# Performance work log

Hardware: AMD Instinct MI355X
Metric: run time of the kernel (lower is better)

## Reference

```python
import jax, jax.numpy as jnp
import numpy as np

B, HF, WF = 64, 14, 14
E, D, H, EM, V, L = 2048, 256, 256, 256, 10000, 32


def setup_inputs() -> dict:
    key = jax.random.key(0)
    ks = jax.random.split(key, 16)
    s = lambda k, shape: jax.random.normal(k, shape, jnp.float32) * 0.02
    lengths = jnp.clip(jax.random.randint(ks[2], (B, 1), 2, L + 1), 2, L)
    lengths = lengths.at[0, 0].set(L)  # ensure max target length == L-1 (static)
    return {
        "image_feature": jax.random.normal(ks[0], (B, HF, WF, E), jnp.float32),
        "caption_token": jax.random.randint(ks[1], (B, L), 0, V),
        "caption_length": lengths,
        "Wf": s(ks[3], (E, H)), "bf": jnp.zeros((H,), jnp.float32),
        "Wh": s(ks[4], (D, H)), "bh": jnp.zeros((H,), jnp.float32),
        "We": s(ks[5], (H, 1)), "be": jnp.zeros((1,), jnp.float32),
        "emb": jax.random.uniform(ks[6], (V, EM), jnp.float32, -0.1, 0.1),
        "W_ih": s(ks[7], (EM + E, 4 * D)), "b_ih": jnp.zeros((4 * D,), jnp.float32),
        "W_hh": s(ks[8], (D, 4 * D)), "b_hh": jnp.zeros((4 * D,), jnp.float32),
        "W_hid": s(ks[9], (E, D)), "b_hid": jnp.zeros((D,), jnp.float32),
        "W_cell": s(ks[10], (E, D)), "b_cell": jnp.zeros((D,), jnp.float32),
        "W_gate": s(ks[11], (D, E)), "b_gate": jnp.zeros((E,), jnp.float32),
        "W_head": jax.random.uniform(ks[12], (D, V), jnp.float32, -0.1, 0.1),
        "b_head": jnp.zeros((V,), jnp.float32),
    }


def reference(image_feature, caption_token, caption_length,
              Wf, bf, Wh, bh, We, be, emb,
              W_ih, b_ih, W_hh, b_hh,
              W_hid, b_hid, W_cell, b_cell,
              W_gate, b_gate, W_head, b_head):
    feat = image_feature.reshape(image_feature.shape[0], -1, image_feature.shape[-1])  # [B,P,E]
    lengths = caption_length[:, 0]
    order = jnp.argsort(-lengths)               # descending, stable
    feat = feat[order]
    tok = caption_token[order]
    target = lengths[order] - 1                 # [B] target lengths
    T = tok.shape[1] - 1                        # static max target length

    mean_feat = feat.mean(axis=1)               # [B,E]
    h0 = mean_feat @ W_hid + b_hid              # init hidden
    c0 = mean_feat @ W_cell + b_cell            # init cell
    cap_emb = emb[tok]                          # [B,L,EM] teacher-forcing embeds
    fe = feat @ Wf + bf                         # [B,P,H] feature proj (loop-invariant)

    def step(carry, t):
        h, c = carry
        m = (target > t)[:, None].astype(h.dtype)        # active-row mask (block_size)
        # additive attention
        he = (h @ Wh + bh)[:, None, :]                   # [B,1,H]
        e = jax.nn.relu(fe + he) @ We + be               # [B,P,1]
        w = jax.nn.softmax(e, axis=1)                    # over pixels
        ctx = (w * feat).sum(axis=1)                     # [B,E]
        # sigmoid gate on context
        ctx = jax.nn.sigmoid(h @ W_gate + b_gate) * ctx
        # LSTMCell (torch gate order i,f,g,o)
        x = jnp.concatenate([cap_emb[:, t], ctx], axis=1)
        g = x @ W_ih + b_ih + h @ W_hh + b_hh
        i, f, gg, o = jnp.split(g, 4, axis=1)
        c_new = jax.nn.sigmoid(f) * c + jax.nn.sigmoid(i) * jnp.tanh(gg)
        h_new = jax.nn.sigmoid(o) * jnp.tanh(c_new)
        pred = h_new @ W_head + b_head                   # dropout = identity (eval)
        h = jnp.where(m > 0, h_new, h)
        c = jnp.where(m > 0, c_new, c)
        return (h, c), (pred * m, w[:, :, 0] * m)

    _, (preds, weights) = jax.lax.scan(step, (h0, c0), jnp.arange(T))
    caption_prediction = jnp.transpose(preds, (1, 0, 2))   # [B,T,V]
    attention_weight = jnp.transpose(weights, (1, 0, 2))   # [B,T,P]
    return caption_prediction, attention_weight
```

## Files before the change

kernel.cpp:

```cpp
#include <hip/hip_runtime.h>
#include <math.h>

#define B 64
#define P 196
#define E 2048
#define D 256
#define H_ 256
#define EM 256
#define V 10000
#define L 32
#define T 31
#define KX 2560

__global__ __launch_bounds__(64) void sort_kernel(const int* __restrict__ clen,
                                                  int* __restrict__ order,
                                                  int* __restrict__ target) {
    __shared__ int len_s[B];
    int i = threadIdx.x;
    len_s[i] = clen[i];
    __syncthreads();
    int li = len_s[i];
    int rank = 0;
    for (int j = 0; j < B; ++j) {
        int lj = len_s[j];
        if (lj > li || (lj == li && j < i)) rank++;
    }
    order[rank] = i;
    target[rank] = li - 1;
}

__global__ __launch_bounds__(256) void mean_kernel(const float* __restrict__ feat,
                                                   const int* __restrict__ order,
                                                   float* __restrict__ mean_feat) {
    int b = blockIdx.x;
    int e = blockIdx.y * 256 + threadIdx.x;
    int src = order[b];
    const float* fp = feat + (size_t)src * P * E + e;
    float acc = 0.f;
    #pragma unroll 4
    for (int p = 0; p < P; ++p) acc += fp[(size_t)p * E];
    mean_feat[b * E + e] = acc * (1.0f / (float)P);
}

__global__ __launch_bounds__(256) void h0c0_gemm(const float* __restrict__ mean_feat,
                                                 const float* __restrict__ W_hid,
                                                 const float* __restrict__ W_cell,
                                                 float* __restrict__ hpart) {
    __shared__ float As[32][68];
    __shared__ float Bs[32][64];
    int cb = blockIdx.x;
    int ky = blockIdx.y;
    int tid = threadIdx.x;
    int tx = tid & 15, ty = tid >> 4;
    const float* Wsrc;
    int ncol0;
    if (cb < 4) { Wsrc = W_hid;  ncol0 = cb * 64; }
    else        { Wsrc = W_cell; ncol0 = (cb - 4) * 64; }
    float acc[4][4] = {};
    for (int k0 = ky * 256; k0 < ky * 256 + 256; k0 += 32) {
        #pragma unroll
        for (int q = 0; q < 2; ++q) {
            int idx = q * 256 + tid;
            int kv = idx & 7, m = idx >> 3;
            float4 v = *(const float4*)(mean_feat + (size_t)m * E + k0 + kv * 4);
            As[kv * 4 + 0][m] = v.x;
            As[kv * 4 + 1][m] = v.y;
            As[kv * 4 + 2][m] = v.z;
            As[kv * 4 + 3][m] = v.w;
        }
        #pragma unroll
        for (int q = 0; q < 2; ++q) {
            int idx = q * 256 + tid;
            int n4 = idx & 15, kk = idx >> 4;
            float4 v = *(const float4*)(Wsrc + (size_t)(k0 + kk) * 256 + ncol0 + n4 * 4);
            *(float4*)&Bs[kk][n4 * 4] = v;
        }
        __syncthreads();
        #pragma unroll
        for (int kk = 0; kk < 32; ++kk) {
            float4 av = *(const float4*)&As[kk][ty * 4];
            float4 bv = *(const float4*)&Bs[kk][tx * 4];
            acc[0][0] += av.x * bv.x; acc[0][1] += av.x * bv.y; acc[0][2] += av.x * bv.z; acc[0][3] += av.x * bv.w;
            acc[1][0] += av.y * bv.x; acc[1][1] += av.y * bv.y; acc[1][2] += av.y * bv.z; acc[1][3] += av.y * bv.w;
            acc[2][0] += av.z * bv.x; acc[2][1] += av.z * bv.y; acc[2][2] += av.z * bv.z; acc[2][3] += av.z * bv.w;
            acc[3][0] += av.w * bv.x; acc[3][1] += av.w * bv.y; acc[3][2] += av.w * bv.z; acc[3][3] += av.w * bv.w;
        }
        __syncthreads();
    }
    #pragma unroll
    for (int a = 0; a < 4; ++a) {
        int row = ty * 4 + a;
        float4 o = {acc[a][0], acc[a][1], acc[a][2], acc[a][3]};
        *(float4*)(hpart + ((size_t)ky * B + row) * 512 + cb * 64 + tx * 4) = o;
    }
}

__global__ __launch_bounds__(256) void h0c0_reduce(const float* __restrict__ hpart,
                                                   const float* __restrict__ b_hid,
                                                   const float* __restrict__ b_cell,
                                                   const float* __restrict__ emb,
                                                   const int* __restrict__ cap_tok,
                                                   const int* __restrict__ order,
                                                   float* __restrict__ h,
                                                   float* __restrict__ c,
                                                   float* __restrict__ xbuf) {
    int b = blockIdx.x, tid = threadIdx.x;
    float s0 = 0.f, s1 = 0.f;
    #pragma unroll
    for (int ky = 0; ky < 8; ++ky) {
        const float* hp = hpart + ((size_t)ky * B + b) * 512;
        s0 += hp[tid];
        s1 += hp[256 + tid];
    }
    float h0 = s0 + b_hid[tid];
    h[b * D + tid] = h0;
    c[b * D + tid] = s1 + b_cell[tid];
    xbuf[(size_t)b * KX + 2304 + tid] = h0;
    int tok0 = cap_tok[order[b] * L + 0];
    xbuf[(size_t)b * KX + tid] = emb[(size_t)tok0 * EM + tid];
}

__global__ __launch_bounds__(256) void fe_gemm(const float* __restrict__ feat,
                                               const int* __restrict__ order,
                                               const float* __restrict__ Wf,
                                               const float* __restrict__ bf,
                                               float* __restrict__ fe) {
    __shared__ float As[32][68];
    __shared__ float Bs[32][64];
    __shared__ int srcRow[64];
    int rowBlock = blockIdx.x;
    int colBlock = blockIdx.y;
    int tid = threadIdx.x;
    if (tid < 64) {
        int gr = rowBlock * 64 + tid;
        int b = gr / P, p = gr % P;
        srcRow[tid] = order[b] * P + p;
    }
    __syncthreads();
    int tx = tid & 15, ty = tid >> 4;
    float acc[4][4] = {};
    for (int k0 = 0; k0 < E; k0 += 32) {
        #pragma unroll
        for (int q = 0; q < 2; ++q) {
            int idx = q * 256 + tid;
            int kv = idx & 7, m = idx >> 3;
            float4 v = *(const float4*)(feat + (size_t)srcRow[m] * E + k0 + kv * 4);
            As[kv * 4 + 0][m] = v.x;
            As[kv * 4 + 1][m] = v.y;
            As[kv * 4 + 2][m] = v.z;
            As[kv * 4 + 3][m] = v.w;
        }
        {
            int n4 = tid & 15, kk = tid >> 4;
            float4 v = *(const float4*)(Wf + (size_t)(k0 + kk) * H_ + colBlock * 64 + n4 * 4);
            *(float4*)&Bs[kk][n4 * 4] = v;
            int kk2 = kk + 16;
            float4 v2 = *(const float4*)(Wf + (size_t)(k0 + kk2) * H_ + colBlock * 64 + n4 * 4);
            *(float4*)&Bs[kk2][n4 * 4] = v2;
        }
        __syncthreads();
        #pragma unroll
        for (int kk = 0; kk < 32; ++kk) {
            float4 av = *(const float4*)&As[kk][ty * 4];
            float4 bv = *(const float4*)&Bs[kk][tx * 4];
            acc[0][0] += av.x * bv.x; acc[0][1] += av.x * bv.y; acc[0][2] += av.x * bv.z; acc[0][3] += av.x * bv.w;
            acc[1][0] += av.y * bv.x; acc[1][1] += av.y * bv.y; acc[1][2] += av.y * bv.z; acc[1][3] += av.y * bv.w;
            acc[2][0] += av.z * bv.x; acc[2][1] += av.z * bv.y; acc[2][2] += av.z * bv.z; acc[2][3] += av.z * bv.w;
            acc[3][0] += av.w * bv.x; acc[3][1] += av.w * bv.y; acc[3][2] += av.w * bv.z; acc[3][3] += av.w * bv.w;
        }
        __syncthreads();
    }
    float4 bias = *(const float4*)(bf + colBlock * 64 + tx * 4);
    #pragma unroll
    for (int a = 0; a < 4; ++a) {
        int gr = rowBlock * 64 + ty * 4 + a;
        float4 o;
        o.x = acc[a][0] + bias.x;
        o.y = acc[a][1] + bias.y;
        o.z = acc[a][2] + bias.z;
        o.w = acc[a][3] + bias.w;
        *(float4*)(fe + (size_t)gr * H_ + colBlock * 64 + tx * 4) = o;
    }
}

__global__ __launch_bounds__(256) void attn_pw(const int* __restrict__ target,
                                               const float* __restrict__ gpart,
                                               const float* __restrict__ b_ih,
                                               const float* __restrict__ b_hh,
                                               const float* __restrict__ emb,
                                               const int* __restrict__ cap_tok,
                                               const int* __restrict__ order,
                                               const float* __restrict__ Wh,
                                               const float* __restrict__ bh,
                                               const float* __restrict__ We,
                                               const float* __restrict__ be,
                                               const float* __restrict__ fe,
                                               float* __restrict__ h,
                                               float* __restrict__ c,
                                               float* __restrict__ hn_all,
                                               float* __restrict__ xbuf,
                                               float* __restrict__ wbuf,
                                               float* __restrict__ out2,
                                               int t) {
    int b = blockIdx.x;
    int tgt = target[b];
    bool pw_active = (t > 0) && (tgt > t - 1);
    bool at_active = (tgt > t);
    if (!pw_active && !at_active) return;
    __shared__ float hs[D];
    __shared__ float hes[D];
    __shared__ float es[P];
    __shared__ float red[4];
    int tid = threadIdx.x;
    if (pw_active) {
        int d = tid;
        float gi = b_ih[d] + b_hh[d];
        float gf = b_ih[D + d] + b_hh[D + d];
        float gg = b_ih[2 * D + d] + b_hh[2 * D + d];
        float go = b_ih[3 * D + d] + b_hh[3 * D + d];
        #pragma unroll
        for (int ky = 0; ky < 8; ++ky) {
            const float* gp = gpart + ((size_t)ky * B + b) * 1024;
            gi += gp[d];
            gf += gp[D + d];
            gg += gp[2 * D + d];
            go += gp[3 * D + d];
        }
        float c_old = c[b * D + d];
        float si = 1.f / (1.f + expf(-gi));
        float sf = 1.f / (1.f + expf(-gf));
        float so = 1.f / (1.f + expf(-go));
        float cn = sf * c_old + si * tanhf(gg);
        float hnv = so * tanhf(cn);
        c[b * D + d] = cn;
        h[b * D + d] = hnv;
        hs[d] = hnv;
        hn_all[((size_t)(t - 1) * B + b) * D + d] = hnv;
        xbuf[(size_t)b * KX + 2304 + d] = hnv;
        int tokn = cap_tok[order[b] * L + t];
        xbuf[(size_t)b * KX + d] = emb[(size_t)tokn * EM + d];
    } else {
        hs[tid] = h[b * D + tid];
    }
    __syncthreads();
    if (!at_active) return;
    float acc = 0.f;
    #pragma unroll 8
    for (int k = 0; k < D; ++k) acc += hs[k] * Wh[(size_t)k * H_ + tid];
    hes[tid] = acc + bh[tid];
    __syncthreads();
    int wave = tid >> 6, lane = tid & 63;
    float4 he4 = *(const float4*)&hes[lane * 4];
    float4 we4 = *(const float4*)(We + lane * 4);
    for (int p = wave; p < P; p += 4) {
        float4 fv = *(const float4*)(fe + ((size_t)b * P + p) * H_ + lane * 4);
        float x0 = fv.x + he4.x; x0 = x0 > 0.f ? x0 : 0.f;
        float x1 = fv.y + he4.y; x1 = x1 > 0.f ? x1 : 0.f;
        float x2 = fv.z + he4.z; x2 = x2 > 0.f ? x2 : 0.f;
        float x3 = fv.w + he4.w; x3 = x3 > 0.f ? x3 : 0.f;
        float s = x0 * we4.x + x1 * we4.y + x2 * we4.z + x3 * we4.w;
        #pragma unroll
        for (int off = 32; off > 0; off >>= 1) s += __shfl_down(s, off);
        if (lane == 0) es[p] = s + be[0];
    }
    __syncthreads();
    float mx = -1e30f;
    for (int p = tid; p < P; p += 256) mx = fmaxf(mx, es[p]);
    #pragma unroll
    for (int off = 32; off > 0; off >>= 1) mx = fmaxf(mx, __shfl_down(mx, off));
    if (lane == 0) red[wave] = mx;
    __syncthreads();
    mx = fmaxf(fmaxf(red[0], red[1]), fmaxf(red[2], red[3]));
    __syncthreads();
    float sum = 0.f;
    for (int p = tid; p < P; p += 256) {
        float ex = expf(es[p] - mx);
        es[p] = ex;
        sum += ex;
    }
    #pragma unroll
    for (int off = 32; off > 0; off >>= 1) sum += __shfl_down(sum, off);
    if (lane == 0) red[wave] = sum;
    __syncthreads();
    sum = red[0] + red[1] + red[2] + red[3];
    float inv = 1.0f / sum;
    for (int p = tid; p < P; p += 256) {
        float wv = es[p] * inv;
        wbuf[b * P + p] = wv;
        out2[((size_t)b * T + t) * P + p] = wv;
    }
}

__global__ __launch_bounds__(256) void ctx_kernel(const float* __restrict__ feat,
                                                  const int* __restrict__ order,
                                                  const float* __restrict__ wbuf,
                                                  const float* __restrict__ W_gate,
                                                  const float* __restrict__ b_gate,
                                                  const float* __restrict__ h,
                                                  const int* __restrict__ target,
                                                  float* __restrict__ xbuf,
                                                  int t) {
    int b = blockIdx.x;
    if (target[b] <= t) return;
    int y = blockIdx.y;
    __shared__ float ws_[P];
    __shared__ float hs[D];
    __shared__ float4 rc[3][64];
    __shared__ float4 rg[3][64];
    int tid = threadIdx.x;
    if (tid < P) ws_[tid] = wbuf[b * P + tid];
    hs[tid] = h[b * D + tid];
    __syncthreads();
    int c4 = tid & 63, q = tid >> 6;
    int src = order[b];
    const float4* f4 = (const float4*)(feat + (size_t)src * P * E) + y * 64 + c4;
    float4 acc = {0.f, 0.f, 0.f, 0.f};
    for (int p = q * 49; p < q * 49 + 49; ++p) {
        float w = ws_[p];
        float4 fv = f4[(size_t)p * 512];
        acc.x += w * fv.x; acc.y += w * fv.y; acc.z += w * fv.z; acc.w += w * fv.w;
    }
    const float4* g4 = (const float4*)W_gate + y * 64 + c4;
    float4 gacc = {0.f, 0.f, 0.f, 0.f};
    for (int k = q * 64; k < q * 64 + 64; ++k) {
        float hv = hs[k];
        float4 wv = g4[(size_t)k * 512];
        gacc.x += hv * wv.x; gacc.y += hv * wv.y; gacc.z += hv * wv.z; gacc.w += hv * wv.w;
    }
    if (q) { rc[q - 1][c4] = acc; rg[q - 1][c4] = gacc; }
    __syncthreads();
    if (q == 0) {
        #pragma unroll
        for (int j = 0; j < 3; ++j) {
            float4 a = rc[j][c4], g = rg[j][c4];
            acc.x += a.x; acc.y += a.y; acc.z += a.z; acc.w += a.w;
            gacc.x += g.x; gacc.y += g.y; gacc.z += g.z; gacc.w += g.w;
        }
        float4 gb = *(const float4*)(b_gate + (y * 64 + c4) * 4);
        float4 o;
        o.x = acc.x / (1.f + expf(-(gacc.x + gb.x)));
        o.y = acc.y / (1.f + expf(-(gacc.y + gb.y)));
        o.z = acc.z / (1.f + expf(-(gacc.z + gb.z)));
        o.w = acc.w / (1.f + expf(-(gacc.w + gb.w)));
        *(float4*)(xbuf + (size_t)b * KX + EM + (y * 64 + c4) * 4) = o;
    }
}

__global__ __launch_bounds__(256) void lstm_gemm(const float* __restrict__ xbuf,
                                                 const float* __restrict__ W_ih,
                                                 const float* __restrict__ W_hh,
                                                 float* __restrict__ gpart) {
    __shared__ float As[32][68];
    __shared__ float Bs[32][64];
    int cb = blockIdx.x;
    int ky = blockIdx.y;
    int tid = threadIdx.x;
    int tx = tid & 15, ty = tid >> 4;
    float acc[4][4] = {};
    int k0base = ky * 320;
    for (int k0 = k0base; k0 < k0base + 320; k0 += 32) {
        #pragma unroll
        for (int q = 0; q < 2; ++q) {
            int idx = q * 256 + tid;
            int kv = idx & 7, m = idx >> 3;
            float4 v = *(const float4*)(xbuf + (size_t)m * KX + k0 + kv * 4);
            As[kv * 4 + 0][m] = v.x;
            As[kv * 4 + 1][m] = v.y;
            As[kv * 4 + 2][m] = v.z;
            As[kv * 4 + 3][m] = v.w;
        }
        #pragma unroll
        for (int q = 0; q < 2; ++q) {
            int idx = q * 256 + tid;
            int n4 = idx & 15, kk = idx >> 4;
            int k = k0 + kk;
            const float* src = (k < EM + E) ? (W_ih + (size_t)k * 1024)
                                            : (W_hh + (size_t)(k - EM - E) * 1024);
            float4 v = *(const float4*)(src + cb * 64 + n4 * 4);
            *(float4*)&Bs[kk][n4 * 4] = v;
        }
        __syncthreads();
        #pragma unroll
        for (int kk = 0; kk < 32; ++kk) {
            float4 av = *(const float4*)&As[kk][ty * 4];
            float4 bv = *(const float4*)&Bs[kk][tx * 4];
            acc[0][0] += av.x * bv.x; acc[0][1] += av.x * bv.y; acc[0][2] += av.x * bv.z; acc[0][3] += av.x * bv.w;
            acc[1][0] += av.y * bv.x; acc[1][1] += av.y * bv.y; acc[1][2] += av.y * bv.z; acc[1][3] += av.y * bv.w;
            acc[2][0] += av.z * bv.x; acc[2][1] += av.z * bv.y; acc[2][2] += av.z * bv.z; acc[2][3] += av.z * bv.w;
            acc[3][0] += av.w * bv.x; acc[3][1] += av.w * bv.y; acc[3][2] += av.w * bv.z; acc[3][3] += av.w * bv.w;
        }
        __syncthreads();
    }
    #pragma unroll
    for (int a = 0; a < 4; ++a) {
        int bidx = ty * 4 + a;
        float4 o = {acc[a][0], acc[a][1], acc[a][2], acc[a][3]};
        *(float4*)(gpart + ((size_t)ky * B + bidx) * 1024 + cb * 64 + tx * 4) = o;
    }
}

__global__ __launch_bounds__(256) void head_batch(const float* __restrict__ hn_all,
                                                  const float* __restrict__ W_head,
                                                  const float* __restrict__ b_head,
                                                  const int* __restrict__ target,
                                                  float* __restrict__ out1) {
    int by = blockIdx.y;
    int t = by >> 1, qh = by & 1;
    if (target[qh * 32] <= t) return;
    __shared__ float hs[32][260];
    int cb = blockIdx.x;
    int tid = threadIdx.x;
    #pragma unroll
    for (int q = 0; q < 8; ++q) {
        int idx = q * 256 + tid;
        int r = idx >> 6, kq = idx & 63;
        float4 v = *(const float4*)(hn_all + ((size_t)t * B + qh * 32 + r) * D + kq * 4);
        *(float4*)&hs[r][kq * 4] = v;
    }
    __syncthreads();
    int col = cb * 64 + (tid & 63);
    int rgrp = (tid >> 6) * 8;
    if (col < V) {
        float acc[8] = {};
        for (int kq = 0; kq < 64; ++kq) {
            float w0 = W_head[(size_t)(kq * 4 + 0) * V + col];
            float w1 = W_head[(size_t)(kq * 4 + 1) * V + col];
            float w2 = W_head[(size_t)(kq * 4 + 2) * V + col];
            float w3 = W_head[(size_t)(kq * 4 + 3) * V + col];
            #pragma unroll
            for (int r = 0; r < 8; ++r) {
                float4 hv = *(const float4*)&hs[rgrp + r][kq * 4];
                acc[r] += hv.x * w0 + hv.y * w1 + hv.z * w2 + hv.w * w3;
            }
        }
        float bh_ = b_head[col];
        #pragma unroll
        for (int r = 0; r < 8; ++r) {
            int brow = qh * 32 + rgrp + r;
            if (target[brow] > t)
                out1[((size_t)brow * T + t) * V + col] = acc[r] + bh_;
        }
    }
}

extern "C" void kernel_launch(void* const* d_in, const int* in_sizes, int n_in,
                              void* d_out, int out_size, void* d_ws, size_t ws_size,
                              hipStream_t stream) {
    const float* feat   = (const float*)d_in[0];
    const int*   tok    = (const int*)d_in[1];
    const int*   clen   = (const int*)d_in[2];
    const float* Wf     = (const float*)d_in[3];
    const float* bf     = (const float*)d_in[4];
    const float* Wh     = (const float*)d_in[5];
    const float* bh     = (const float*)d_in[6];
    const float* We     = (const float*)d_in[7];
    const float* be     = (const float*)d_in[8];
    const float* emb    = (const float*)d_in[9];
    const float* W_ih   = (const float*)d_in[10];
    const float* b_ih   = (const float*)d_in[11];
    const float* W_hh   = (const float*)d_in[12];
    const float* b_hh   = (const float*)d_in[13];
    const float* W_hid  = (const float*)d_in[14];
    const float* b_hid  = (const float*)d_in[15];
    const float* W_cell = (const float*)d_in[16];
    const float* b_cell = (const float*)d_in[17];
    const float* W_gate = (const float*)d_in[18];
    const float* b_gate = (const float*)d_in[19];
    const float* W_head = (const float*)d_in[20];
    const float* b_head = (const float*)d_in[21];

    float* out1 = (float*)d_out;
    float* out2 = out1 + (size_t)B * T * V;

    char* wp = (char*)d_ws;
    int* order   = (int*)wp;           wp += 256;
    int* targetp = (int*)wp;           wp += 256;
    float* fe    = (float*)wp;         wp += (size_t)B * P * H_ * sizeof(float);
    float* hbuf  = (float*)wp;         wp += (size_t)B * D * sizeof(float);
    float* cbuf  = (float*)wp;         wp += (size_t)B * D * sizeof(float);
    float* wbuf  = (float*)wp;         wp += (size_t)B * P * sizeof(float);
    float* xbuf  = (float*)wp;         wp += (size_t)B * KX * sizeof(float);
    float* gpart = (float*)wp;         wp += (size_t)8 * B * 1024 * sizeof(float);
    float* mean_feat = (float*)wp;     wp += (size_t)B * E * sizeof(float);
    float* hpart = (float*)wp;         wp += (size_t)8 * B * 512 * sizeof(float);
    float* hn_all = (float*)wp;        wp += (size_t)T * B * D * sizeof(float);

    hipMemsetAsync(d_out, 0, (size_t)out_size * sizeof(float), stream);

    sort_kernel<<<1, 64, 0, stream>>>(clen, order, targetp);
    mean_kernel<<<dim3(B, E / 256), 256, 0, stream>>>(feat, order, mean_feat);
    h0c0_gemm<<<dim3(8, 8), 256, 0, stream>>>(mean_feat, W_hid, W_cell, hpart);
    h0c0_reduce<<<B, 256, 0, stream>>>(hpart, b_hid, b_cell, emb, tok, order,
                                       hbuf, cbuf, xbuf);
    fe_gemm<<<dim3(196, 4), 256, 0, stream>>>(feat, order, Wf, bf, fe);

    for (int t = 0; t < T; ++t) {
        attn_pw<<<B, 256, 0, stream>>>(targetp, gpart, b_ih, b_hh, emb, tok, order,
                                       Wh, bh, We, be, fe, hbuf, cbuf, hn_all,
                                       xbuf, wbuf, out2, t);
        ctx_kernel<<<dim3(B, 8), 256, 0, stream>>>(feat, order, wbuf, W_gate, b_gate,
                                                   hbuf, targetp, xbuf, t);
        lstm_gemm<<<dim3(16, 8), 256, 0, stream>>>(xbuf, W_ih, W_hh, gpart);
    }
    attn_pw<<<B, 256, 0, stream>>>(targetp, gpart, b_ih, b_hh, emb, tok, order,
                                   Wh, bh, We, be, fe, hbuf, cbuf, hn_all,
                                   xbuf, wbuf, out2, T);
    head_batch<<<dim3(157, 62), 256, 0, stream>>>(hn_all, W_head, b_head, targetp, out1);
}
```

Before: 2.848 ms.

## Fuse recurrent time loop into one persistent cooperative kernel with grid syncs

Replaces the 94 per-timestep kernel launches (attention/pointwise, context, LSTM GEMM) with a single cooperative persistent kernel of 512 blocks that runs all phases and separates them with grid-wide barriers. This targets launch overhead and inter-kernel gaps in the latency-bound recurrence. It adds grid.sync costs, requires all 512 blocks to be co-resident, and keeps the old multi-launch path as a fallback if the cooperative launch fails.

```diff
diff --git a/kernel.cpp b/kernel.cpp
--- a/kernel.cpp
+++ b/kernel.cpp
@@ -1,5 +1,8 @@
 #include <hip/hip_runtime.h>
+#include <hip/hip_cooperative_groups.h>
 #include <math.h>
+
+namespace cg = cooperative_groups;
 
 #define B 64
 #define P 196
@@ -399,6 +402,227 @@
     }
 }
 
+__global__ __launch_bounds__(256, 2) void loop_kernel(
+        const int* __restrict__ target,
+        float* __restrict__ gpart,
+        const float* __restrict__ b_ih,
+        const float* __restrict__ b_hh,
+        const float* __restrict__ emb,
+        const int* __restrict__ cap_tok,
+        const int* __restrict__ order,
+        const float* __restrict__ Wh,
+        const float* __restrict__ bh,
+        const float* __restrict__ We,
+        const float* __restrict__ be,
+        const float* __restrict__ fe,
+        float* __restrict__ h,
+        float* __restrict__ c,
+        float* __restrict__ hn_all,
+        float* __restrict__ xbuf,
+        float* __restrict__ wbuf,
+        float* __restrict__ out2,
+        const float* __restrict__ feat,
+        const float* __restrict__ W_gate,
+        const float* __restrict__ b_gate,
+        const float* __restrict__ W_ih,
+        const float* __restrict__ W_hh) {
+    cg::grid_group grid = cg::this_grid();
+    __shared__ __align__(16) char smem_raw[17408];
+    int bid = blockIdx.x;
+    int tid = threadIdx.x;
+
+    for (int t = 0; ; ++t) {
+        if (bid < B) {
+            float* hs  = (float*)smem_raw;
+            float* hes = hs + 256;
+            float* es  = hes + 256;
+            float* red = es + 200;
+            int b = bid;
+            int tgt = target[b];
+            bool pw_active = (t > 0) && (tgt > t - 1);
+            bool at_active = (t < T) && (tgt > t);
+            if (pw_active || at_active) {
+                if (pw_active) {
+                    int d = tid;
+                    float gi = b_ih[d] + b_hh[d];
+                    float gf = b_ih[D + d] + b_hh[D + d];
+                    float gg = b_ih[2 * D + d] + b_hh[2 * D + d];
+                    float go = b_ih[3 * D + d] + b_hh[3 * D + d];
+                    #pragma unroll
+                    for (int ky = 0; ky < 8; ++ky) {
+                        const float* gp = gpart + ((size_t)ky * B + b) * 1024;
+                        gi += gp[d];
+                        gf += gp[D + d];
+                        gg += gp[2 * D + d];
+                        go += gp[3 * D + d];
+                    }
+                    float c_old = c[b * D + d];
+                    float si = 1.f / (1.f + expf(-gi));
+                    float sf = 1.f / (1.f + expf(-gf));
+                    float so = 1.f / (1.f + expf(-go));
+                    float cn = sf * c_old + si * tanhf(gg);
+                    float hnv = so * tanhf(cn);
+                    c[b * D + d] = cn;
+                    h[b * D + d] = hnv;
+                    hs[d] = hnv;
+                    hn_all[((size_t)(t - 1) * B + b) * D + d] = hnv;
+                    xbuf[(size_t)b * KX + 2304 + d] = hnv;
+                    int tokn = cap_tok[order[b] * L + t];
+                    xbuf[(size_t)b * KX + d] = emb[(size_t)tokn * EM + d];
+                } else {
+                    hs[tid] = h[b * D + tid];
+                }
+                __syncthreads();
+                if (at_active) {
+                    float acc = 0.f;
+                    #pragma unroll 8
+                    for (int k = 0; k < D; ++k) acc += hs[k] * Wh[(size_t)k * H_ + tid];
+                    hes[tid] = acc + bh[tid];
+                    __syncthreads();
+                    int wave = tid >> 6, lane = tid & 63;
+                    float4 he4 = *(const float4*)&hes[lane * 4];
+                    float4 we4 = *(const float4*)(We + lane * 4);
+                    for (int p = wave; p < P; p += 4) {
+                        float4 fv = *(const float4*)(fe + ((size_t)b * P + p) * H_ + lane * 4);
+                        float x0 = fv.x + he4.x; x0 = x0 > 0.f ? x0 : 0.f;
+                        float x1 = fv.y + he4.y; x1 = x1 > 0.f ? x1 : 0.f;
+                        float x2 = fv.z + he4.z; x2 = x2 > 0.f ? x2 : 0.f;
+                        float x3 = fv.w + he4.w; x3 = x3 > 0.f ? x3 : 0.f;
+                        float s = x0 * we4.x + x1 * we4.y + x2 * we4.z + x3 * we4.w;
+                        #pragma unroll
+                        for (int off = 32; off > 0; off >>= 1) s += __shfl_down(s, off);
+                        if (lane == 0) es[p] = s + be[0];
+                    }
+                    __syncthreads();
+                    float mx = -1e30f;
+                    for (int p = tid; p < P; p += 256) mx = fmaxf(mx, es[p]);
+                    #pragma unroll
+                    for (int off = 32; off > 0; off >>= 1) mx = fmaxf(mx, __shfl_down(mx, off));
+                    if (lane == 0) red[wave] = mx;
+                    __syncthreads();
+                    mx = fmaxf(fmaxf(red[0], red[1]), fmaxf(red[2], red[3]));
+                    __syncthreads();
+                    float sum = 0.f;
+                    for (int p = tid; p < P; p += 256) {
+                        float ex = expf(es[p] - mx);
+                        es[p] = ex;
+                        sum += ex;
+                    }
+                    #pragma unroll
+                    for (int off = 32; off > 0; off >>= 1) sum += __shfl_down(sum, off);
+                    if (lane == 0) red[wave] = sum;
+                    __syncthreads();
+                    sum = red[0] + red[1] + red[2] + red[3];
+                    float inv = 1.0f / sum;
+                    for (int p = tid; p < P; p += 256) {
+                        float wv = es[p] * inv;
+                        wbuf[b * P + p] = wv;
+                        out2[((size_t)b * T + t) * P + p] = wv;
+                    }
+                }
+            }
+        }
+        if (t == T) break;
+        grid.sync();
+
+        {
+            int b = bid >> 3, y = bid & 7;
+            if (target[b] > t) {
+                float*  ws_ = (float*)smem_raw;
+                float*  hsB = ws_ + 200;
+                float4* rc  = (float4*)(smem_raw + 1824);
+                float4* rg  = rc + 192;
+                if (tid < P) ws_[tid] = wbuf[b * P + tid];
+                hsB[tid] = h[b * D + tid];
+                __syncthreads();
+                int c4 = tid & 63, q = tid >> 6;
+                int src = order[b];
+                const float4* f4 = (const float4*)(feat + (size_t)src * P * E) + y * 64 + c4;
+                float4 acc = {0.f, 0.f, 0.f, 0.f};
+                for (int p = q * 49; p < q * 49 + 49; ++p) {
+                    float w = ws_[p];
+                    float4 fv = f4[(size_t)p * 512];
+                    acc.x += w * fv.x; acc.y += w * fv.y; acc.z += w * fv.z; acc.w += w * fv.w;
+                }
+                const float4* g4 = (const float4*)W_gate + y * 64 + c4;
+                float4 gacc = {0.f, 0.f, 0.f, 0.f};
+                for (int k = q * 64; k < q * 64 + 64; ++k) {
+                    float hv = hsB[k];
+                    float4 wv = g4[(size_t)k * 512];
+                    gacc.x += hv * wv.x; gacc.y += hv * wv.y; gacc.z += hv * wv.z; gacc.w += hv * wv.w;
+                }
+                if (q) { rc[(q - 1) * 64 + c4] = acc; rg[(q - 1) * 64 + c4] = gacc; }
+                __syncthreads();
+                if (q == 0) {
+                    #pragma unroll
+                    for (int j = 0; j < 3; ++j) {
+                        float4 a = rc[j * 64 + c4], g = rg[j * 64 + c4];
+                        acc.x += a.x; acc.y += a.y; acc.z += a.z; acc.w += a.w;
+                        gacc.x += g.x; gacc.y += g.y; gacc.z += g.z; gacc.w += g.w;
+                    }
+                    float4 gb = *(const float4*)(b_gate + (y * 64 + c4) * 4);
+                    float4 o;
+                    o.x = acc.x / (1.f + expf(-(gacc.x + gb.x)));
+                    o.y = acc.y / (1.f + expf(-(gacc.y + gb.y)));
+                    o.z = acc.z / (1.f + expf(-(gacc.z + gb.z)));
+                    o.w = acc.w / (1.f + expf(-(gacc.w + gb.w)));
+                    *(float4*)(xbuf + (size_t)b * KX + EM + (y * 64 + c4) * 4) = o;
+                }
+            }
+        }
+        grid.sync();
+
+        if (bid < 128) {
+            float (*As)[68] = (float (*)[68])smem_raw;
+            float (*Bs)[64] = (float (*)[64])(smem_raw + 8704);
+            int cb = bid & 15, ky = bid >> 4;
+            int tx = tid & 15, ty = tid >> 4;
+            float acc[4][4] = {};
+            int k0base = ky * 320;
+            for (int k0 = k0base; k0 < k0base + 320; k0 += 32) {
+                #pragma unroll
+                for (int q = 0; q < 2; ++q) {
+                    int idx = q * 256 + tid;
+                    int kv = idx & 7, m = idx >> 3;
+                    float4 v = *(const float4*)(xbuf + (size_t)m * KX + k0 + kv * 4);
+                    As[kv * 4 + 0][m] = v.x;
+                    As[kv * 4 + 1][m] = v.y;
+                    As[kv * 4 + 2][m] = v.z;
+                    As[kv * 4 + 3][m] = v.w;
+                }
+                #pragma unroll
+                for (int q = 0; q < 2; ++q) {
+                    int idx = q * 256 + tid;
+                    int n4 = idx & 15, kk = idx >> 4;
+                    int k = k0 + kk;
+                    const float* src = (k < EM + E) ? (W_ih + (size_t)k * 1024)
+                                                    : (W_hh + (size_t)(k - EM - E) * 1024);
+                    float4 v = *(const float4*)(src + cb * 64 + n4 * 4);
+                    *(float4*)&Bs[kk][n4 * 4] = v;
+                }
+                __syncthreads();
+                #pragma unroll
+                for (int kk = 0; kk < 32; ++kk) {
+                    float4 av = *(const float4*)&As[kk][ty * 4];
+                    float4 bv = *(const float4*)&Bs[kk][tx * 4];
+                    acc[0][0] += av.x * bv.x; acc[0][1] += av.x * bv.y; acc[0][2] += av.x * bv.z; acc[0][3] += av.x * bv.w;
+                    acc[1][0] += av.y * bv.x; acc[1][1] += av.y * bv.y; acc[1][2] += av.y * bv.z; acc[1][3] += av.y * bv.w;
+                    acc[2][0] += av.z * bv.x; acc[2][1] += av.z * bv.y; acc[2][2] += av.z * bv.z; acc[2][3] += av.z * bv.w;
+                    acc[3][0] += av.w * bv.x; acc[3][1] += av.w * bv.y; acc[3][2] += av.w * bv.z; acc[3][3] += av.w * bv.w;
+                }
+                __syncthreads();
+            }
+            #pragma unroll
+            for (int a = 0; a < 4; ++a) {
+                int bidx = ty * 4 + a;
+                float4 o = {acc[a][0], acc[a][1], acc[a][2], acc[a][3]};
+                *(float4*)(gpart + ((size_t)ky * B + bidx) * 1024 + cb * 64 + tx * 4) = o;
+            }
+        }
+        grid.sync();
+    }
+}
+
 __global__ __launch_bounds__(256) void head_batch(const float* __restrict__ hn_all,
                                                   const float* __restrict__ W_head,
                                                   const float* __restrict__ b_head,
@@ -494,16 +718,29 @@
                                        hbuf, cbuf, xbuf);
     fe_gemm<<<dim3(196, 4), 256, 0, stream>>>(feat, order, Wf, bf, fe);
 
-    for (int t = 0; t < T; ++t) {
+    void* kargs[] = {
+        (void*)&targetp, (void*)&gpart, (void*)&b_ih, (void*)&b_hh,
+        (void*)&emb, (void*)&tok, (void*)&order, (void*)&Wh, (void*)&bh,
+        (void*)&We, (void*)&be, (void*)&fe, (void*)&hbuf, (void*)&cbuf,
+        (void*)&hn_all, (void*)&xbuf, (void*)&wbuf, (void*)&out2,
+        (void*)&feat, (void*)&W_gate, (void*)&b_gate, (void*)&W_ih, (void*)&W_hh
+    };
+    hipError_t cerr = hipLaunchCooperativeKernel((const void*)loop_kernel,
+                                                 dim3(512), dim3(256),
+                                                 kargs, 0, stream);
+    if (cerr != hipSuccess) {
+        for (int t = 0; t < T; ++t) {
+            attn_pw<<<B, 256, 0, stream>>>(targetp, gpart, b_ih, b_hh, emb, tok, order,
+                                           Wh, bh, We, be, fe, hbuf, cbuf, hn_all,
+                                           xbuf, wbuf, out2, t);
+            ctx_kernel<<<dim3(B, 8), 256, 0, stream>>>(feat, order, wbuf, W_gate, b_gate,
+                                                       hbuf, targetp, xbuf, t);
+            lstm_gemm<<<dim3(16, 8), 256, 0, stream>>>(xbuf, W_ih, W_hh, gpart);
+        }
         attn_pw<<<B, 256, 0, stream>>>(targetp, gpart, b_ih, b_hh, emb, tok, order,
                                        Wh, bh, We, be, fe, hbuf, cbuf, hn_all,
-                                       xbuf, wbuf, out2, t);
-        ctx_kernel<<<dim3(B, 8), 256, 0, stream>>>(feat, order, wbuf, W_gate, b_gate,
-                                                   hbuf, targetp, xbuf, t);
-        lstm_gemm<<<dim3(16, 8), 256, 0, stream>>>(xbuf, W_ih, W_hh, gpart);
-    }
-    attn_pw<<<B, 256, 0, stream>>>(targetp, gpart, b_ih, b_hh, emb, tok, order,
-                                   Wh, bh, We, be, fe, hbuf, cbuf, hn_all,
-                                   xbuf, wbuf, out2, T);
+                                       xbuf, wbuf, out2, T);
+    }
+
     head_batch<<<dim3(157, 62), 256, 0, stream>>>(hn_all, W_head, b_head, targetp, out1);
 }
```

After: 10.61 ms. 273% more time.

## Fuse attention and context kernels per step with double-buffered cell state

Applied to the files above, without the earlier changes.

Merges the per-step attention/LSTM-pointwise kernel and the context/gate kernel into one kernel launched on a (batch, 8) grid. Each of the 8 column blocks recomputes the pointwise update, the Wh projection and the softmax so the attention weights stay in shared memory instead of going through a global buffer. The cell state is double-buffered across steps to avoid races between blocks, and a small final pointwise kernel replaces the last attention launch. This removes one launch and a global round-trip per step, but repeats the Wh matvec and the fe reads eight times per batch row.

```diff
diff --git a/kernel.cpp b/kernel.cpp
--- a/kernel.cpp
+++ b/kernel.cpp
@@ -102,7 +102,7 @@
                                                    const int* __restrict__ cap_tok,
                                                    const int* __restrict__ order,
                                                    float* __restrict__ h,
-                                                   float* __restrict__ c,
+                                                   float* __restrict__ c0,
                                                    float* __restrict__ xbuf) {
     int b = blockIdx.x, tid = threadIdx.x;
     float s0 = 0.f, s1 = 0.f;
@@ -114,7 +114,7 @@
     }
     float h0 = s0 + b_hid[tid];
     h[b * D + tid] = h0;
-    c[b * D + tid] = s1 + b_cell[tid];
+    c0[b * D + tid] = s1 + b_cell[tid];
     xbuf[(size_t)b * KX + 2304 + tid] = h0;
     int tok0 = cap_tok[order[b] * L + 0];
     xbuf[(size_t)b * KX + tid] = emb[(size_t)tok0 * EM + tid];
@@ -183,35 +183,41 @@
     }
 }
 
-__global__ __launch_bounds__(256) void attn_pw(const int* __restrict__ target,
-                                               const float* __restrict__ gpart,
-                                               const float* __restrict__ b_ih,
-                                               const float* __restrict__ b_hh,
-                                               const float* __restrict__ emb,
-                                               const int* __restrict__ cap_tok,
-                                               const int* __restrict__ order,
-                                               const float* __restrict__ Wh,
-                                               const float* __restrict__ bh,
-                                               const float* __restrict__ We,
-                                               const float* __restrict__ be,
-                                               const float* __restrict__ fe,
-                                               float* __restrict__ h,
-                                               float* __restrict__ c,
-                                               float* __restrict__ hn_all,
-                                               float* __restrict__ xbuf,
-                                               float* __restrict__ wbuf,
-                                               float* __restrict__ out2,
-                                               int t) {
-    int b = blockIdx.x;
+__global__ __launch_bounds__(256) void attn_ctx(const int* __restrict__ target,
+                                                const float* __restrict__ gpart,
+                                                const float* __restrict__ b_ih,
+                                                const float* __restrict__ b_hh,
+                                                const float* __restrict__ emb,
+                                                const int* __restrict__ cap_tok,
+                                                const int* __restrict__ order,
+                                                const float* __restrict__ Wh,
+                                                const float* __restrict__ bh,
+                                                const float* __restrict__ We,
+                                                const float* __restrict__ be,
+                                                const float* __restrict__ fe,
+                                                const float* __restrict__ h0,
+                                                const float* __restrict__ c_rd,
+                                                float* __restrict__ c_wr,
+                                                float* __restrict__ hn_all,
+                                                float* __restrict__ xbuf,
+                                                float* __restrict__ out2,
+                                                const float* __restrict__ feat,
+                                                const float* __restrict__ W_gate,
+                                                const float* __restrict__ b_gate,
+                                                int t) {
+    int b = blockIdx.x, y = blockIdx.y, tid = threadIdx.x;
     int tgt = target[b];
     bool pw_active = (t > 0) && (tgt > t - 1);
     bool at_active = (tgt > t);
-    if (!pw_active && !at_active) return;
+    if (!at_active && !(pw_active && y == 0)) return;
+
     __shared__ float hs[D];
     __shared__ float hes[D];
-    __shared__ float es[P];
+    __shared__ float es[200];
     __shared__ float red[4];
-    int tid = threadIdx.x;
+    __shared__ float4 rc[3][64];
+    __shared__ float4 rg[3][64];
+
     if (pw_active) {
         int d = tid;
         float gi = b_ih[d] + b_hh[d];
@@ -226,124 +232,146 @@
             gg += gp[2 * D + d];
             go += gp[3 * D + d];
         }
-        float c_old = c[b * D + d];
+        float c_old = c_rd[b * D + d];
         float si = 1.f / (1.f + expf(-gi));
         float sf = 1.f / (1.f + expf(-gf));
         float so = 1.f / (1.f + expf(-go));
         float cn = sf * c_old + si * tanhf(gg);
         float hnv = so * tanhf(cn);
-        c[b * D + d] = cn;
-        h[b * D + d] = hnv;
         hs[d] = hnv;
-        hn_all[((size_t)(t - 1) * B + b) * D + d] = hnv;
-        xbuf[(size_t)b * KX + 2304 + d] = hnv;
-        int tokn = cap_tok[order[b] * L + t];
-        xbuf[(size_t)b * KX + d] = emb[(size_t)tokn * EM + d];
+        if (y == 0) {
+            c_wr[b * D + d] = cn;
+            hn_all[((size_t)(t - 1) * B + b) * D + d] = hnv;
+            xbuf[(size_t)b * KX + 2304 + d] = hnv;
+            int tokn = cap_tok[order[b] * L + t];
+            xbuf[(size_t)b * KX + d] = emb[(size_t)tokn * EM + d];
+        }
     } else {
-        hs[tid] = h[b * D + tid];
+        hs[tid] = h0[b * D + tid];
     }
     __syncthreads();
     if (!at_active) return;
-    float acc = 0.f;
-    #pragma unroll 8
-    for (int k = 0; k < D; ++k) acc += hs[k] * Wh[(size_t)k * H_ + tid];
-    hes[tid] = acc + bh[tid];
-    __syncthreads();
+
+    {
+        float acc = 0.f;
+        #pragma unroll 8
+        for (int k = 0; k < D; ++k) acc += hs[k] * Wh[(size_t)k * H_ + tid];
+        hes[tid] = acc + bh[tid];
+    }
+    __syncthreads();
+
     int wave = tid >> 6, lane = tid & 63;
-    float4 he4 = *(const float4*)&hes[lane * 4];
-    float4 we4 = *(const float4*)(We + lane * 4);
-    for (int p = wave; p < P; p += 4) {
-        float4 fv = *(const float4*)(fe + ((size_t)b * P + p) * H_ + lane * 4);
-        float x0 = fv.x + he4.x; x0 = x0 > 0.f ? x0 : 0.f;
-        float x1 = fv.y + he4.y; x1 = x1 > 0.f ? x1 : 0.f;
-        float x2 = fv.z + he4.z; x2 = x2 > 0.f ? x2 : 0.f;
-        float x3 = fv.w + he4.w; x3 = x3 > 0.f ? x3 : 0.f;
-        float s = x0 * we4.x + x1 * we4.y + x2 * we4.z + x3 * we4.w;
-        #pragma unroll
-        for (int off = 32; off > 0; off >>= 1) s += __shfl_down(s, off);
-        if (lane == 0) es[p] = s + be[0];
-    }
-    __syncthreads();
-    float mx = -1e30f;
-    for (int p = tid; p < P; p += 256) mx = fmaxf(mx, es[p]);
+    {
+        float4 he4 = *(const float4*)&hes[lane * 4];
+        float4 we4 = *(const float4*)(We + lane * 4);
+        for (int p = wave; p < P; p += 4) {
+            float4 fv = *(const float4*)(fe + ((size_t)b * P + p) * H_ + lane * 4);
+            float x0 = fv.x + he4.x; x0 = x0 > 0.f ? x0 : 0.f;
+            float x1 = fv.y + he4.y; x1 = x1 > 0.f ? x1 : 0.f;
+            float x2 = fv.z + he4.z; x2 = x2 > 0.f ? x2 : 0.f;
+            float x3 = fv.w + he4.w; x3 = x3 > 0.f ? x3 : 0.f;
+            float s = x0 * we4.x + x1 * we4.y + x2 * we4.z + x3 * we4.w;
+            #pragma unroll
+            for (int off = 32; off > 0; off >>= 1) s += __shfl_down(s, off);
+            if (lane == 0) es[p] = s + be[0];
+        }
+    }
+    __syncthreads();
+
+    {
+        float mx = -1e30f;
+        for (int p = tid; p < P; p += 256) mx = fmaxf(mx, es[p]);
+        #pragma unroll
+        for (int off = 32; off > 0; off >>= 1) mx = fmaxf(mx, __shfl_down(mx, off));
+        if (lane == 0) red[wave] = mx;
+        __syncthreads();
+        mx = fmaxf(fmaxf(red[0], red[1]), fmaxf(red[2], red[3]));
+        __syncthreads();
+        float sum = 0.f;
+        for (int p = tid; p < P; p += 256) {
+            float ex = expf(es[p] - mx);
+            es[p] = ex;
+            sum += ex;
+        }
+        #pragma unroll
+        for (int off = 32; off > 0; off >>= 1) sum += __shfl_down(sum, off);
+        if (lane == 0) red[wave] = sum;
+        __syncthreads();
+        sum = red[0] + red[1] + red[2] + red[3];
+        float inv = 1.0f / sum;
+        for (int p = tid; p < P; p += 256) {
+            float wv = es[p] * inv;
+            es[p] = wv;
+            if (y == 0) out2[((size_t)b * T + t) * P + p] = wv;
+        }
+    }
+    __syncthreads();
+
+    {
+        int c4 = tid & 63, q = tid >> 6;
+        int src = order[b];
+        const float4* f4 = (const float4*)(feat + (size_t)src * P * E) + y * 64 + c4;
+        float4 acc = {0.f, 0.f, 0.f, 0.f};
+        for (int p = q * 49; p < q * 49 + 49; ++p) {
+            float w = es[p];
+            float4 fv = f4[(size_t)p * 512];
+            acc.x += w * fv.x; acc.y += w * fv.y; acc.z += w * fv.z; acc.w += w * fv.w;
+        }
+        const float4* g4 = (const float4*)W_gate + y * 64 + c4;
+        float4 gacc = {0.f, 0.f, 0.f, 0.f};
+        for (int k = q * 64; k < q * 64 + 64; ++k) {
+            float hv = hs[k];
+            float4 wv = g4[(size_t)k * 512];
+            gacc.x += hv * wv.x; gacc.y += hv * wv.y; gacc.z += hv * wv.z; gacc.w += hv * wv.w;
+        }
+        if (q) { rc[q - 1][c4] = acc; rg[q - 1][c4] = gacc; }
+        __syncthreads();
+        if (q == 0) {
+            #pragma unroll
+            for (int j = 0; j < 3; ++j) {
+                float4 a = rc[j][c4], g = rg[j][c4];
+                acc.x += a.x; acc.y += a.y; acc.z += a.z; acc.w += a.w;
+                gacc.x += g.x; gacc.y += g.y; gacc.z += g.z; gacc.w += g.w;
+            }
+            float4 gb = *(const float4*)(b_gate + (y * 64 + c4) * 4);
+            float4 o;
+            o.x = acc.x / (1.f + expf(-(gacc.x + gb.x)));
+            o.y = acc.y / (1.f + expf(-(gacc.y + gb.y)));
+            o.z = acc.z / (1.f + expf(-(gacc.z + gb.z)));
+            o.w = acc.w / (1.f + expf(-(gacc.w + gb.w)));
+            *(float4*)(xbuf + (size_t)b * KX + EM + (y * 64 + c4) * 4) = o;
+        }
+    }
+}
+
+__global__ __launch_bounds__(256) void pw_final(const int* __restrict__ target,
+                                                const float* __restrict__ gpart,
+                                                const float* __restrict__ b_ih,
+                                                const float* __restrict__ b_hh,
+                                                const float* __restrict__ c_rd,
+                                                float* __restrict__ hn_all) {
+    int b = blockIdx.x;
+    if (target[b] < T) return;
+    int d = threadIdx.x;
+    float gi = b_ih[d] + b_hh[d];
+    float gf = b_ih[D + d] + b_hh[D + d];
+    float gg = b_ih[2 * D + d] + b_hh[2 * D + d];
+    float go = b_ih[3 * D + d] + b_hh[3 * D + d];
     #pragma unroll
-    for (int off = 32; off > 0; off >>= 1) mx = fmaxf(mx, __shfl_down(mx, off));
-    if (lane == 0) red[wave] = mx;
-    __syncthreads();
-    mx = fmaxf(fmaxf(red[0], red[1]), fmaxf(red[2], red[3]));
-    __syncthreads();
-    float sum = 0.f;
-    for (int p = tid; p < P; p += 256) {
-        float ex = expf(es[p] - mx);
-        es[p] = ex;
-        sum += ex;
-    }
-    #pragma unroll
-    for (int off = 32; off > 0; off >>= 1) sum += __shfl_down(sum, off);
-    if (lane == 0) red[wave] = sum;
-    __syncthreads();
-    sum = red[0] + red[1] + red[2] + red[3];
-    float inv = 1.0f / sum;
-    for (int p = tid; p < P; p += 256) {
-        float wv = es[p] * inv;
-        wbuf[b * P + p] = wv;
-        out2[((size_t)b * T + t) * P + p] = wv;
-    }
-}
-
-__global__ __launch_bounds__(256) void ctx_kernel(const float* __restrict__ feat,
-                                                  const int* __restrict__ order,
-                                                  const float* __restrict__ wbuf,
-                                                  const float* __restrict__ W_gate,
-                                                  const float* __restrict__ b_gate,
-                                                  const float* __restrict__ h,
-                                                  const int* __restrict__ target,
-                                                  float* __restrict__ xbuf,
-                                                  int t) {
-    int b = blockIdx.x;
-    if (target[b] <= t) return;
-    int y = blockIdx.y;
-    __shared__ float ws_[P];
-    __shared__ float hs[D];
-    __shared__ float4 rc[3][64];
-    __shared__ float4 rg[3][64];
-    int tid = threadIdx.x;
-    if (tid < P) ws_[tid] = wbuf[b * P + tid];
-    hs[tid] = h[b * D + tid];
-    __syncthreads();
-    int c4 = tid & 63, q = tid >> 6;
-    int src = order[b];
-    const float4* f4 = (const float4*)(feat + (size_t)src * P * E) + y * 64 + c4;
-    float4 acc = {0.f, 0.f, 0.f, 0.f};
-    for (int p = q * 49; p < q * 49 + 49; ++p) {
-        float w = ws_[p];
-        float4 fv = f4[(size_t)p * 512];
-        acc.x += w * fv.x; acc.y += w * fv.y; acc.z += w * fv.z; acc.w += w * fv.w;
-    }
-    const float4* g4 = (const float4*)W_gate + y * 64 + c4;
-    float4 gacc = {0.f, 0.f, 0.f, 0.f};
-    for (int k = q * 64; k < q * 64 + 64; ++k) {
-        float hv = hs[k];
-        float4 wv = g4[(size_t)k * 512];
-        gacc.x += hv * wv.x; gacc.y += hv * wv.y; gacc.z += hv * wv.z; gacc.w += hv * wv.w;
-    }
-    if (q) { rc[q - 1][c4] = acc; rg[q - 1][c4] = gacc; }
-    __syncthreads();
-    if (q == 0) {
-        #pragma unroll
-        for (int j = 0; j < 3; ++j) {
-            float4 a = rc[j][c4], g = rg[j][c4];
-            acc.x += a.x; acc.y += a.y; acc.z += a.z; acc.w += a.w;
-            gacc.x += g.x; gacc.y += g.y; gacc.z += g.z; gacc.w += g.w;
-        }
-        float4 gb = *(const float4*)(b_gate + (y * 64 + c4) * 4);
-        float4 o;
-        o.x = acc.x / (1.f + expf(-(gacc.x + gb.x)));
-        o.y = acc.y / (1.f + expf(-(gacc.y + gb.y)));
-        o.z = acc.z / (1.f + expf(-(gacc.z + gb.z)));
-        o.w = acc.w / (1.f + expf(-(gacc.w + gb.w)));
-        *(float4*)(xbuf + (size_t)b * KX + EM + (y * 64 + c4) * 4) = o;
-    }
+    for (int ky = 0; ky < 8; ++ky) {
+        const float* gp = gpart + ((size_t)ky * B + b) * 1024;
+        gi += gp[d];
+        gf += gp[D + d];
+        gg += gp[2 * D + d];
+        go += gp[3 * D + d];
+    }
+    float c_old = c_rd[b * D + d];
+    float si = 1.f / (1.f + expf(-gi));
+    float sf = 1.f / (1.f + expf(-gf));
+    float so = 1.f / (1.f + expf(-go));
+    float cn = sf * c_old + si * tanhf(gg);
+    float hnv = so * tanhf(cn);
+    hn_all[((size_t)(T - 1) * B + b) * D + d] = hnv;
 }
 
 __global__ __launch_bounds__(256) void lstm_gemm(const float* __restrict__ xbuf,
@@ -477,8 +505,7 @@
     int* targetp = (int*)wp;           wp += 256;
     float* fe    = (float*)wp;         wp += (size_t)B * P * H_ * sizeof(float);
     float* hbuf  = (float*)wp;         wp += (size_t)B * D * sizeof(float);
-    float* cbuf  = (float*)wp;         wp += (size_t)B * D * sizeof(float);
-    float* wbuf  = (float*)wp;         wp += (size_t)B * P * sizeof(float);
+    float* cbuf  = (float*)wp;         wp += (size_t)2 * B * D * sizeof(float);
     float* xbuf  = (float*)wp;         wp += (size_t)B * KX * sizeof(float);
     float* gpart = (float*)wp;         wp += (size_t)8 * B * 1024 * sizeof(float);
     float* mean_feat = (float*)wp;     wp += (size_t)B * E * sizeof(float);
@@ -495,15 +522,15 @@
     fe_gemm<<<dim3(196, 4), 256, 0, stream>>>(feat, order, Wf, bf, fe);
 
     for (int t = 0; t < T; ++t) {
-        attn_pw<<<B, 256, 0, stream>>>(targetp, gpart, b_ih, b_hh, emb, tok, order,
-                                       Wh, bh, We, be, fe, hbuf, cbuf, hn_all,
-                                       xbuf, wbuf, out2, t);
-        ctx_kernel<<<dim3(B, 8), 256, 0, stream>>>(feat, order, wbuf, W_gate, b_gate,
-                                                   hbuf, targetp, xbuf, t);
+        attn_ctx<<<dim3(B, 8), 256, 0, stream>>>(targetp, gpart, b_ih, b_hh, emb, tok,
+                                                 order, Wh, bh, We, be, fe, hbuf,
+                                                 cbuf + (size_t)((t + 1) & 1) * B * D,
+                                                 cbuf + (size_t)(t & 1) * B * D,
+                                                 hn_all, xbuf, out2,
+                                                 feat, W_gate, b_gate, t);
         lstm_gemm<<<dim3(16, 8), 256, 0, stream>>>(xbuf, W_ih, W_hh, gpart);
     }
-    attn_pw<<<B, 256, 0, stream>>>(targetp, gpart, b_ih, b_hh, emb, tok, order,
-                                   Wh, bh, We, be, fe, hbuf, cbuf, hn_all,
-                                   xbuf, wbuf, out2, T);
+    pw_final<<<B, 256, 0, stream>>>(targetp, gpart, b_ih, b_hh, cbuf, hn_all);
+
     head_batch<<<dim3(157, 62), 256, 0, stream>>>(hn_all, W_head, b_head, targetp, out1);
 }
```

After: 2.732 ms. 1.04x faster.
